# Performance work log

Measured on AMD Instinct MI355X. Metric: run time of the kernel, lower is better.

## Reference

```python
import jax, jax.numpy as jnp
import numpy as np

DIM = 1024        # BIGNET_DIM
GROUP = 16        # Linear4Bit group_size
LORA = 20         # lora_dim hardcoded in Block
NLAYERS = 18      # 6 blocks * 3 QLoRALinear
NBLOCKS = 6
BATCH = 8192
EPS = 1e-5


def setup_inputs() -> dict:
    key = jax.random.key(0)
    ks = jax.random.split(key, 6)
    x = jax.random.normal(ks[0], (BATCH, DIM), jnp.float32)
    # int4 quantized base weights in [-8, 7], stored as int32
    qw = jax.random.randint(ks[1], (NLAYERS, DIM, DIM), -8, 8, jnp.int32)
    # per-(out_row, input-group) dequant scales
    scales = jax.random.uniform(ks[2], (NLAYERS, DIM, DIM // GROUP), jnp.float32,
                                minval=0.005, maxval=0.02)
    bias = jax.random.normal(ks[3], (NLAYERS, DIM), jnp.float32) * 0.01
    # lora_a: kaiming-uniform-like scale; lora_b: small nonzero (zeros in torch init,
    # randomized here so the LoRA path is numerically exercised)
    lora_a = jax.random.normal(ks[4], (NLAYERS, LORA, DIM), jnp.float32) / np.sqrt(DIM)
    lora_b = jax.random.normal(ks[5], (NLAYERS, DIM, LORA), jnp.float32) * 0.01
    ln_w = jnp.ones((NBLOCKS - 1, DIM), jnp.float32)
    ln_b = jnp.zeros((NBLOCKS - 1, DIM), jnp.float32)
    return dict(x=x, qw=qw, scales=scales, bias=bias,
                lora_a=lora_a, lora_b=lora_b, ln_w=ln_w, ln_b=ln_b)


def _qlora_linear(x, qw, sc, b, A, B):
    # dequantize: each group of 16 input cols of a row shares one scale
    w = (qw.astype(jnp.float32).reshape(DIM, DIM // GROUP, GROUP)
         * sc[:, :, None]).reshape(DIM, DIM)          # [out, in]
    base = x @ w.T + b                                # [N, out]
    lora = (x @ A.T) @ B.T                            # [N, r] @ [r, out]
    return base + lora


def _layernorm(x, w, b):
    m = jnp.mean(x, axis=-1, keepdims=True)
    v = jnp.mean((x - m) ** 2, axis=-1, keepdims=True)
    return (x - m) * jax.lax.rsqrt(v + EPS) * w + b


def reference(x, qw, scales, bias, lora_a, lora_b, ln_w, ln_b):
    h = x
    li = 0
    for blk in range(NBLOCKS):
        r = h
        for j in range(3):
            r = _qlora_linear(r, qw[li], scales[li], bias[li], lora_a[li], lora_b[li])
            if j < 2:
                r = jax.nn.relu(r)
            li += 1
        h = h + r  # residual
        if blk < NBLOCKS - 1:
            h = _layernorm(h, ln_w[blk], ln_b[blk])
    return h
```

## Files before the change

### kernel.cpp

```cpp
#include <hip/hip_runtime.h>
#include <cstdint>
#include <cstddef>

#define DIM      1024
#define GROUP    16
#define LORA     20
#define NLAYERS  18
#define NBLOCKS  6
#define BATCH    8192
#define EPS      1e-5f

typedef __bf16 bf16_8 __attribute__((ext_vector_type(8)));
typedef __bf16 bf16_4 __attribute__((ext_vector_type(4)));
typedef float  f32x4  __attribute__((ext_vector_type(4)));

__global__ __launch_bounds__(256, 2) void wprep_kernel(
    const int* __restrict__ qw, const float* __restrict__ sc,
    const float* __restrict__ la, const float* __restrict__ lb,
    __bf16* __restrict__ whi) {
  const int l  = blockIdx.x >> 7;
  const int og = (blockIdx.x >> 1) & 63;
  const int cg = blockIdx.x & 1;
  const int tid = threadIdx.x;

  __shared__ float As[10 * 512];
  __shared__ float Bs[16 * LORA];

  const float* Abase = la + (size_t)l * LORA * DIM + cg * 512;
  const float* Bbase = lb + ((size_t)l * DIM + og * 16) * LORA;
  for (int i = tid; i < 16 * LORA; i += 256) Bs[i] = Bbase[i];
#pragma unroll
  for (int i = 0; i < 5; ++i) {
    const int f4 = i * 256 + tid;
    ((float4*)As)[f4] = *(const float4*)(Abase + (size_t)(f4 >> 7) * DIM + (f4 & 127) * 4);
  }
  __syncthreads();

  const int tc = tid & 31;
  const int tr = tid >> 5;

  float acc[2][16];
  size_t rowb[2];
#pragma unroll
  for (int u = 0; u < 2; ++u) {
    const int orow = og * 16 + tr * 2 + u;
    rowb[u] = ((size_t)l * DIM + orow) * DIM + cg * 512;
    const size_t scb = ((size_t)l * DIM + orow) * (DIM / GROUP) + cg * 32;
#pragma unroll
    for (int v = 0; v < 4; ++v) {
      const int c = v * 128 + tc * 4;
      const int4 q4 = *(const int4*)&qw[rowb[u] + c];
      const float sv = sc[scb + (c >> 4)];
      acc[u][v * 4 + 0] = q4.x * sv;
      acc[u][v * 4 + 1] = q4.y * sv;
      acc[u][v * 4 + 2] = q4.z * sv;
      acc[u][v * 4 + 3] = q4.w * sv;
    }
  }

#pragma unroll 1
  for (int half = 0; half < 2; ++half) {
    if (half == 1) {
      __syncthreads();
#pragma unroll
      for (int i = 0; i < 5; ++i) {
        const int f4 = i * 256 + tid;
        ((float4*)As)[f4] =
            *(const float4*)(Abase + (size_t)(10 + (f4 >> 7)) * DIM + (f4 & 127) * 4);
      }
      __syncthreads();
    }
#pragma unroll 2
    for (int jj = 0; jj < 10; ++jj) {
      const int j = half * 10 + jj;
      float4 a[4];
#pragma unroll
      for (int v = 0; v < 4; ++v)
        a[v] = *(const float4*)&As[jj * 512 + v * 128 + tc * 4];
#pragma unroll
      for (int u = 0; u < 2; ++u) {
        const float bj = Bs[(tr * 2 + u) * LORA + j];
#pragma unroll
        for (int v = 0; v < 4; ++v) {
          acc[u][v * 4 + 0] += bj * a[v].x;
          acc[u][v * 4 + 1] += bj * a[v].y;
          acc[u][v * 4 + 2] += bj * a[v].z;
          acc[u][v * 4 + 3] += bj * a[v].w;
        }
      }
    }
  }

#pragma unroll
  for (int u = 0; u < 2; ++u) {
#pragma unroll
    for (int v = 0; v < 4; ++v) {
      const bf16_4 hv = {(__bf16)acc[u][v * 4 + 0], (__bf16)acc[u][v * 4 + 1],
                         (__bf16)acc[u][v * 4 + 2], (__bf16)acc[u][v * 4 + 3]};
      *(bf16_4*)&whi[rowb[u] + v * 128 + tc * 4] = hv;
    }
  }
}

__global__ __launch_bounds__(256) void xprep_kernel(
    const float* __restrict__ x, __bf16* __restrict__ hi) {
  const size_t i = (size_t)blockIdx.x * 256 + threadIdx.x;
  const float4 v = ((const float4*)x)[i];
  const bf16_4 hv = {(__bf16)v.x, (__bf16)v.y, (__bf16)v.z, (__bf16)v.w};
  ((bf16_4*)hi)[i] = hv;
}

#define GBUF    12288
#define GOFF_W  8192

template <int NISSUE>
__device__ __forceinline__ void stageR(const __bf16* __restrict__ g, int row0, int k0,
                                       __bf16* lds, int tid) {
#pragma unroll
  for (int i = 0; i < NISSUE; ++i) {
    const int D = i * 8192 + tid * 16;
    const int r  = D >> 6;
    const int ce = (D & 63) >> 1;
    const __bf16* gp = g + (size_t)(row0 + r) * DIM + k0 + ce;
    __builtin_amdgcn_global_load_lds(
        (const __attribute__((address_space(1))) void*)gp,
        (__attribute__((address_space(3))) void*)(lds + i * 4096 + (tid >> 6) * 512), 16, 0, 0);
  }
}

template <bool RELU_OUT>
__global__ __launch_bounds__(512, 1) void gemm1_kernel(
    const __bf16* __restrict__ X, const __bf16* __restrict__ Wh,
    const float* __restrict__ bias, __bf16* __restrict__ Oh,
    const float* __restrict__ Hin, float* __restrict__ Sout) {
  __shared__ __bf16 smem[3 * GBUF];

  const int tid  = threadIdx.x;
  const int lane = tid & 63;
  const int wv   = tid >> 6;
  const int wm   = wv >> 2;
  const int wn2  = wv & 3;
  const int xcd = blockIdx.x & 7;
  const int kk  = blockIdx.x >> 3;
  const int tm  = xcd * 4 + (kk >> 3);
  const int tn  = kk & 7;
  const int rowX = tm * 256, rowW = tn * 128;

  const int lr   = lane & 15;
  const int slot = lane >> 4;

  int offX[4], offW[4];
#pragma unroll
  for (int n = 0; n < 4; ++n) offX[n] = (wn2 * 64 + n * 16 + lr) * 32 + slot * 8;
#pragma unroll
  for (int m = 0; m < 4; ++m) offW[m] = GOFF_W + (wm * 64 + m * 16 + lr) * 32 + slot * 8;

  f32x4 acc[4][4];
#pragma unroll
  for (int m = 0; m < 4; ++m)
#pragma unroll
    for (int n = 0; n < 4; ++n) acc[m][n] = f32x4{0.f, 0.f, 0.f, 0.f};

  auto stage_tile = [&](int k0, __bf16* sb) {
    stageR<2>(X,  rowX, k0, sb, tid);
    stageR<1>(Wh, rowW, k0, sb + GOFF_W, tid);
  };

  auto compute_tile = [&](const __bf16* buf) {
    bf16_8 xf[4];
#pragma unroll
    for (int n = 0; n < 4; ++n) xf[n] = *(const bf16_8*)&buf[offX[n]];
#pragma unroll
    for (int m = 0; m < 4; ++m) {
      const bf16_8 w_h = *(const bf16_8*)&buf[offW[m]];
#pragma unroll
      for (int n = 0; n < 4; ++n)
        acc[m][n] = __builtin_amdgcn_mfma_f32_16x16x32_bf16(w_h, xf[n], acc[m][n], 0, 0, 0);
    }
  };

  stage_tile(0, smem);
  stage_tile(32, smem + GBUF);
  asm volatile("s_waitcnt vmcnt(3)" ::: "memory");
  __builtin_amdgcn_s_barrier();

  int cur = 0;
#pragma unroll 1
  for (int kt = 0; kt < 30; ++kt) {
    int pb = cur + 2; if (pb >= 3) pb -= 3;
    stage_tile((kt + 2) * 32, smem + pb * GBUF);
    compute_tile(smem + cur * GBUF);
    asm volatile("s_waitcnt vmcnt(3)" ::: "memory");
    __builtin_amdgcn_s_barrier();
    ++cur; if (cur == 3) cur = 0;
  }
  compute_tile(smem + cur * GBUF);
  asm volatile("s_waitcnt vmcnt(0)" ::: "memory");
  __builtin_amdgcn_s_barrier();
  ++cur; if (cur == 3) cur = 0;
  compute_tile(smem + cur * GBUF);

  const int g4 = slot * 4;
#pragma unroll
  for (int m = 0; m < 4; ++m) {
    const int feat = tn * 128 + wm * 64 + m * 16 + g4;
    const float4 bv = *(const float4*)&bias[feat];
#pragma unroll
    for (int n = 0; n < 4; ++n) {
      const int nb = tm * 256 + wn2 * 64 + n * 16 + lr;
      const size_t base = (size_t)nb * DIM + feat;
      float v0 = acc[m][n][0] + bv.x;
      float v1 = acc[m][n][1] + bv.y;
      float v2 = acc[m][n][2] + bv.z;
      float v3 = acc[m][n][3] + bv.w;
      if constexpr (RELU_OUT) {
        const bf16_4 hv = {(__bf16)fmaxf(v0, 0.f), (__bf16)fmaxf(v1, 0.f),
                           (__bf16)fmaxf(v2, 0.f), (__bf16)fmaxf(v3, 0.f)};
        *(bf16_4*)&Oh[base] = hv;
      } else {
        const float4 h = *(const float4*)&Hin[base];
        *(float4*)&Sout[base] = float4{v0 + h.x, v1 + h.y, v2 + h.z, v3 + h.w};
      }
    }
  }
}

__global__ __launch_bounds__(256) void ln_kernel(
    const float* __restrict__ S, const float* __restrict__ w,
    const float* __restrict__ b, float* __restrict__ H,
    __bf16* __restrict__ phi) {
  const int row = blockIdx.x;
  const int tid = threadIdx.x;
  const int lane = tid & 63;
  const int wv = tid >> 6;
  const float4 v = ((const float4*)(S + (size_t)row * DIM))[tid];

  float s = v.x + v.y + v.z + v.w;
#pragma unroll
  for (int m = 32; m; m >>= 1) s += __shfl_xor(s, m, 64);
  __shared__ float red[8];
  if (lane == 0) red[wv] = s;
  __syncthreads();
  const float mean = (red[0] + red[1] + red[2] + red[3]) * (1.f / DIM);

  const float d0 = v.x - mean, d1 = v.y - mean, d2 = v.z - mean, d3 = v.w - mean;
  float q = d0 * d0 + d1 * d1 + d2 * d2 + d3 * d3;
#pragma unroll
  for (int m = 32; m; m >>= 1) q += __shfl_xor(q, m, 64);
  if (lane == 0) red[4 + wv] = q;
  __syncthreads();
  const float var = (red[4] + red[5] + red[6] + red[7]) * (1.f / DIM);
  const float inv = 1.f / sqrtf(var + EPS);

  const float4 wv4 = ((const float4*)w)[tid];
  const float4 bv4 = ((const float4*)b)[tid];
  const float y0 = d0 * inv * wv4.x + bv4.x;
  const float y1 = d1 * inv * wv4.y + bv4.y;
  const float y2 = d2 * inv * wv4.z + bv4.z;
  const float y3 = d3 * inv * wv4.w + bv4.w;

  ((float4*)(H + (size_t)row * DIM))[tid] = float4{y0, y1, y2, y3};
  const bf16_4 hv = {(__bf16)y0, (__bf16)y1, (__bf16)y2, (__bf16)y3};
  ((bf16_4*)phi)[(size_t)row * (DIM / 4) + tid] = hv;
}

extern "C" void kernel_launch(void* const* d_in, const int* in_sizes, int n_in,
                              void* d_out, int out_size, void* d_ws, size_t ws_size,
                              hipStream_t stream) {
  const float* x   = (const float*)d_in[0];
  const int*   qw  = (const int*)d_in[1];
  const float* sc  = (const float*)d_in[2];
  const float* bias= (const float*)d_in[3];
  const float* la  = (const float*)d_in[4];
  const float* lb  = (const float*)d_in[5];
  const float* lnw = (const float*)d_in[6];
  const float* lnb = (const float*)d_in[7];
  float* out = (float*)d_out;
  char* ws = (char*)d_ws;

  __bf16* WHI = (__bf16*)(ws);
  __bf16* X0  = (__bf16*)(ws + 37748736);
  __bf16* X1  = (__bf16*)(ws + 54525952);
  float*  Sb  = (float*)(ws + 71303168);
  float*  Hb  = (float*)(ws + 104857600);
  (void)ws_size; (void)in_sizes; (void)n_in; (void)out_size;

  xprep_kernel<<<BATCH * DIM / (256 * 4), 256, 0, stream>>>(x, X0);
  wprep_kernel<<<NLAYERS * 128, 256, 0, stream>>>(qw, sc, la, lb, WHI);

  const dim3 ggrid(BATCH / 256 * (DIM / 128));
  for (int blk = 0; blk < NBLOCKS; ++blk) {
    const int li = blk * 3;
    const size_t w0 = (size_t)li * DIM * DIM;
    const size_t w1 = (size_t)(li + 1) * DIM * DIM;
    const size_t w2 = (size_t)(li + 2) * DIM * DIM;

    gemm1_kernel<true><<<ggrid, 512, 0, stream>>>(
        X0, WHI + w0, bias + (size_t)li * DIM, X1, nullptr, nullptr);
    gemm1_kernel<true><<<ggrid, 512, 0, stream>>>(
        X1, WHI + w1, bias + (size_t)(li + 1) * DIM, X0, nullptr, nullptr);
    const float* hin = (blk == 0) ? x : Hb;
    float* sout = (blk == NBLOCKS - 1) ? out : Sb;
    gemm1_kernel<false><<<ggrid, 512, 0, stream>>>(
        X0, WHI + w2, bias + (size_t)(li + 2) * DIM, nullptr, hin, sout);
    if (blk < NBLOCKS - 1) {
      ln_kernel<<<BATCH, 256, 0, stream>>>(Sb, lnw + (size_t)blk * DIM,
                                           lnb + (size_t)blk * DIM, Hb, X0);
    }
  }
}
```

Baseline: 579.4 us.

## Deepen GEMM LDS pipeline to six stages and fuse LayerNorm apply into residual epilogue

The GEMM moves from a three-buffer to a six-buffer LDS ring in dynamic shared memory. It stages two k-tiles ahead per iteration and computes two per barrier, so the number of barriers is halved and more loads are in flight. The LayerNorm kernel no longer writes the full fp32 normalized H. It writes per-row (mean, inv) stats plus the bf16 activations, and the residual GEMM epilogue recomputes the normalized value from the previous sum buffer. This cuts fp32 write traffic, but needs 144KB of dynamic LDS per block, and launches without raising the dynamic-LDS attribute may fail if the default limit is lower.

Result: slower. 603.8 us (+4.2%).

```diff
diff --git a/kernel.cpp b/kernel.cpp
--- a/kernel.cpp
+++ b/kernel.cpp
@@ -128,12 +128,15 @@
   }
 }
 
-template <bool RELU_OUT>
+template <int MODE>
 __global__ __launch_bounds__(512, 1) void gemm1_kernel(
     const __bf16* __restrict__ X, const __bf16* __restrict__ Wh,
     const float* __restrict__ bias, __bf16* __restrict__ Oh,
-    const float* __restrict__ Hin, float* __restrict__ Sout) {
-  __shared__ __bf16 smem[3 * GBUF];
+    const float* __restrict__ Hin,
+    const float2* __restrict__ stats,
+    const float* __restrict__ lnw, const float* __restrict__ lnb,
+    float* __restrict__ Sout) {
+  extern __shared__ __bf16 smem[];
 
   const int tid  = threadIdx.x;
   const int lane = tid & 63;
@@ -161,12 +164,14 @@
 #pragma unroll
     for (int n = 0; n < 4; ++n) acc[m][n] = f32x4{0.f, 0.f, 0.f, 0.f};
 
-  auto stage_tile = [&](int k0, __bf16* sb) {
-    stageR<2>(X,  rowX, k0, sb, tid);
-    stageR<1>(Wh, rowW, k0, sb + GOFF_W, tid);
+  auto stage_tile = [&](int t) {
+    __bf16* sb = smem + (t % 6) * GBUF;
+    stageR<2>(X,  rowX, t * 32, sb, tid);
+    stageR<1>(Wh, rowW, t * 32, sb + GOFF_W, tid);
   };
 
-  auto compute_tile = [&](const __bf16* buf) {
+  auto compute_tile = [&](int t) {
+    const __bf16* buf = smem + (t % 6) * GBUF;
     bf16_8 xf[4];
 #pragma unroll
     for (int n = 0; n < 4; ++n) xf[n] = *(const bf16_8*)&buf[offX[n]];
@@ -179,32 +184,36 @@
     }
   };
 
-  stage_tile(0, smem);
-  stage_tile(32, smem + GBUF);
-  asm volatile("s_waitcnt vmcnt(3)" ::: "memory");
+  stage_tile(0); stage_tile(1); stage_tile(2); stage_tile(3);
+  asm volatile("s_waitcnt vmcnt(6)" ::: "memory");
   __builtin_amdgcn_s_barrier();
 
-  int cur = 0;
 #pragma unroll 1
-  for (int kt = 0; kt < 30; ++kt) {
-    int pb = cur + 2; if (pb >= 3) pb -= 3;
-    stage_tile((kt + 2) * 32, smem + pb * GBUF);
-    compute_tile(smem + cur * GBUF);
-    asm volatile("s_waitcnt vmcnt(3)" ::: "memory");
+  for (int kt = 0; kt < 28; kt += 2) {
+    stage_tile(kt + 4);
+    stage_tile(kt + 5);
+    compute_tile(kt);
+    compute_tile(kt + 1);
+    asm volatile("s_waitcnt vmcnt(6)" ::: "memory");
     __builtin_amdgcn_s_barrier();
-    ++cur; if (cur == 3) cur = 0;
-  }
-  compute_tile(smem + cur * GBUF);
+  }
+  compute_tile(28);
+  compute_tile(29);
   asm volatile("s_waitcnt vmcnt(0)" ::: "memory");
   __builtin_amdgcn_s_barrier();
-  ++cur; if (cur == 3) cur = 0;
-  compute_tile(smem + cur * GBUF);
+  compute_tile(30);
+  compute_tile(31);
 
   const int g4 = slot * 4;
 #pragma unroll
   for (int m = 0; m < 4; ++m) {
     const int feat = tn * 128 + wm * 64 + m * 16 + g4;
     const float4 bv = *(const float4*)&bias[feat];
+    float4 wq, bq;
+    if constexpr (MODE == 2) {
+      wq = *(const float4*)&lnw[feat];
+      bq = *(const float4*)&lnb[feat];
+    }
 #pragma unroll
     for (int n = 0; n < 4; ++n) {
       const int nb = tm * 256 + wn2 * 64 + n * 16 + lr;
@@ -213,21 +222,29 @@
       float v1 = acc[m][n][1] + bv.y;
       float v2 = acc[m][n][2] + bv.z;
       float v3 = acc[m][n][3] + bv.w;
-      if constexpr (RELU_OUT) {
+      if constexpr (MODE == 0) {
         const bf16_4 hv = {(__bf16)fmaxf(v0, 0.f), (__bf16)fmaxf(v1, 0.f),
                            (__bf16)fmaxf(v2, 0.f), (__bf16)fmaxf(v3, 0.f)};
         *(bf16_4*)&Oh[base] = hv;
-      } else {
+      } else if constexpr (MODE == 1) {
         const float4 h = *(const float4*)&Hin[base];
         *(float4*)&Sout[base] = float4{v0 + h.x, v1 + h.y, v2 + h.z, v3 + h.w};
+      } else {
+        const float2 st = stats[nb];
+        const float4 s = *(const float4*)&Hin[base];
+        const float h0 = (s.x - st.x) * st.y * wq.x + bq.x;
+        const float h1 = (s.y - st.x) * st.y * wq.y + bq.y;
+        const float h2 = (s.z - st.x) * st.y * wq.z + bq.z;
+        const float h3 = (s.w - st.x) * st.y * wq.w + bq.w;
+        *(float4*)&Sout[base] = float4{v0 + h0, v1 + h1, v2 + h2, v3 + h3};
       }
     }
   }
 }
 
-__global__ __launch_bounds__(256) void ln_kernel(
+__global__ __launch_bounds__(256) void normcast_kernel(
     const float* __restrict__ S, const float* __restrict__ w,
-    const float* __restrict__ b, float* __restrict__ H,
+    const float* __restrict__ b, float2* __restrict__ stats,
     __bf16* __restrict__ phi) {
   const int row = blockIdx.x;
   const int tid = threadIdx.x;
@@ -252,15 +269,14 @@
   const float var = (red[4] + red[5] + red[6] + red[7]) * (1.f / DIM);
   const float inv = 1.f / sqrtf(var + EPS);
 
+  if (tid == 0) stats[row] = float2{mean, inv};
+
   const float4 wv4 = ((const float4*)w)[tid];
   const float4 bv4 = ((const float4*)b)[tid];
-  const float y0 = d0 * inv * wv4.x + bv4.x;
-  const float y1 = d1 * inv * wv4.y + bv4.y;
-  const float y2 = d2 * inv * wv4.z + bv4.z;
-  const float y3 = d3 * inv * wv4.w + bv4.w;
-
-  ((float4*)(H + (size_t)row * DIM))[tid] = float4{y0, y1, y2, y3};
-  const bf16_4 hv = {(__bf16)y0, (__bf16)y1, (__bf16)y2, (__bf16)y3};
+  const bf16_4 hv = {(__bf16)(d0 * inv * wv4.x + bv4.x),
+                     (__bf16)(d1 * inv * wv4.y + bv4.y),
+                     (__bf16)(d2 * inv * wv4.z + bv4.z),
+                     (__bf16)(d3 * inv * wv4.w + bv4.w)};
   ((bf16_4*)phi)[(size_t)row * (DIM / 4) + tid] = hv;
 }
 
@@ -281,31 +297,44 @@
   __bf16* WHI = (__bf16*)(ws);
   __bf16* X0  = (__bf16*)(ws + 37748736);
   __bf16* X1  = (__bf16*)(ws + 54525952);
-  float*  Sb  = (float*)(ws + 71303168);
-  float*  Hb  = (float*)(ws + 104857600);
+  float*  SA  = (float*)(ws + 71303168);
+  float*  SB  = (float*)(ws + 104857600);
+  float2* STT = (float2*)(ws + 138412032);
   (void)ws_size; (void)in_sizes; (void)n_in; (void)out_size;
 
   xprep_kernel<<<BATCH * DIM / (256 * 4), 256, 0, stream>>>(x, X0);
   wprep_kernel<<<NLAYERS * 128, 256, 0, stream>>>(qw, sc, la, lb, WHI);
 
   const dim3 ggrid(BATCH / 256 * (DIM / 128));
+  const size_t smem_bytes = 6 * GBUF * sizeof(__bf16);
   for (int blk = 0; blk < NBLOCKS; ++blk) {
     const int li = blk * 3;
     const size_t w0 = (size_t)li * DIM * DIM;
     const size_t w1 = (size_t)(li + 1) * DIM * DIM;
     const size_t w2 = (size_t)(li + 2) * DIM * DIM;
-
-    gemm1_kernel<true><<<ggrid, 512, 0, stream>>>(
-        X0, WHI + w0, bias + (size_t)li * DIM, X1, nullptr, nullptr);
-    gemm1_kernel<true><<<ggrid, 512, 0, stream>>>(
-        X1, WHI + w1, bias + (size_t)(li + 1) * DIM, X0, nullptr, nullptr);
-    const float* hin = (blk == 0) ? x : Hb;
-    float* sout = (blk == NBLOCKS - 1) ? out : Sb;
-    gemm1_kernel<false><<<ggrid, 512, 0, stream>>>(
-        X0, WHI + w2, bias + (size_t)(li + 2) * DIM, nullptr, hin, sout);
+    float* Scur = (blk & 1) ? SB : SA;
+    float* Sprev = (blk & 1) ? SA : SB;
+
+    gemm1_kernel<0><<<ggrid, 512, smem_bytes, stream>>>(
+        X0, WHI + w0, bias + (size_t)li * DIM, X1,
+        nullptr, nullptr, nullptr, nullptr, nullptr);
+    gemm1_kernel<0><<<ggrid, 512, smem_bytes, stream>>>(
+        X1, WHI + w1, bias + (size_t)(li + 1) * DIM, X0,
+        nullptr, nullptr, nullptr, nullptr, nullptr);
+    float* sout = (blk == NBLOCKS - 1) ? out : Scur;
+    if (blk == 0) {
+      gemm1_kernel<1><<<ggrid, 512, smem_bytes, stream>>>(
+          X0, WHI + w2, bias + (size_t)(li + 2) * DIM, nullptr,
+          x, nullptr, nullptr, nullptr, sout);
+    } else {
+      gemm1_kernel<2><<<ggrid, 512, smem_bytes, stream>>>(
+          X0, WHI + w2, bias + (size_t)(li + 2) * DIM, nullptr,
+          Sprev, STT, lnw + (size_t)(blk - 1) * DIM, lnb + (size_t)(blk - 1) * DIM,
+          sout);
+    }
     if (blk < NBLOCKS - 1) {
-      ln_kernel<<<BATCH, 256, 0, stream>>>(Sb, lnw + (size_t)blk * DIM,
-                                           lnb + (size_t)blk * DIM, Hb, X0);
-    }
-  }
-}
+      normcast_kernel<<<BATCH, 256, 0, stream>>>(
+          Scur, lnw + (size_t)blk * DIM, lnb + (size_t)blk * DIM, STT, X0);
+    }
+  }
+}
```
